# Optimization experiments

Measured on AMD Instinct MI355X. Metric: run time of the kernel, lower is better.

## Reference

```python
import jax, jax.numpy as jnp
import numpy as np

N_NODES = 100000
N_EDGES = 1600000
HIDDEN = 128
OUT_DIM = 1
N_GRAPHS = 2048
VOCAB = 28  # atom types, Embedding(28, hidden_dim)


def setup_inputs() -> dict:
    key = jax.random.key(0)
    ks = jax.random.split(key, 14)
    s = 1.0 / np.sqrt(HIDDEN)
    inp = {
        "x_idx": jax.random.randint(ks[0], (N_NODES,), 0, VOCAB, dtype=jnp.int32),
        "edge_src": jax.random.randint(ks[1], (N_EDGES,), 0, N_NODES, dtype=jnp.int32),
        "edge_dst": jax.random.randint(ks[2], (N_EDGES,), 0, N_NODES, dtype=jnp.int32),
        "batch": jnp.sort(jax.random.randint(ks[3], (N_NODES,), 0, N_GRAPHS, dtype=jnp.int32)),
        # parameters
        "embed": jax.random.normal(ks[4], (VOCAB, HIDDEN), dtype=jnp.float32) * 0.02,
        "eps0": jnp.zeros((1,), dtype=jnp.float32),
        "w1_0": jax.random.normal(ks[5], (HIDDEN, HIDDEN), dtype=jnp.float32) * s,
        "b1_0": jnp.zeros((HIDDEN,), dtype=jnp.float32),
        "w2_0": jax.random.normal(ks[6], (HIDDEN, HIDDEN), dtype=jnp.float32) * s,
        "b2_0": jnp.zeros((HIDDEN,), dtype=jnp.float32),
        "eps1": jnp.zeros((1,), dtype=jnp.float32),
        "w1_1": jax.random.normal(ks[7], (HIDDEN, HIDDEN), dtype=jnp.float32) * s,
        "b1_1": jnp.zeros((HIDDEN,), dtype=jnp.float32),
        "w2_1": jax.random.normal(ks[8], (HIDDEN, OUT_DIM), dtype=jnp.float32) * s,
        "b2_1": jnp.zeros((OUT_DIM,), dtype=jnp.float32),
    }
    return inp


def _gin_layer(x, edge_src, edge_dst, eps, w1, b1, w2, b2):
    # A @ x via edge-list SpMM: out[dst] += x[src]  (same math as to_dense().matmul(x))
    agg = jax.ops.segment_sum(x[edge_src], edge_dst, num_segments=N_NODES)
    h = agg + (1.0 + eps) * x  # [N, in_feats]; eps broadcasts (shape [1])
    h = h @ w1 + b1            # linear1 (no nonlinearity between, as in source)
    return h @ w2 + b2         # linear2


def reference(x_idx, edge_src, edge_dst, batch, embed,
              eps0, w1_0, b1_0, w2_0, b2_0,
              eps1, w1_1, b1_1, w2_1, b2_1):
    x = embed[x_idx]  # [N, HIDDEN] — Embedding lookup (.squeeze(1) trivial here)
    x = jax.nn.relu(_gin_layer(x, edge_src, edge_dst, eps0, w1_0, b1_0, w2_0, b2_0))
    x = _gin_layer(x, edge_src, edge_dst, eps1, w1_1, b1_1, w2_1, b2_1)  # [N, 1]
    y_hat = jax.ops.segment_sum(x.squeeze(-1), batch, num_segments=N_GRAPHS)  # [G]
    return (y_hat, x)
```

## Files before the change

### kernel.cpp

```cpp
#include <hip/hip_runtime.h>

#define N_NODES  100000
#define N_EDGES  1600000
#define HIDDEN   128
#define N_GRAPHS 2048
#define VOCAB    28
#define NB       512
#define NPB      196
#define CAP      3600
#define NBIN     512
#define EPB      3125
#define EPT      4
#define CSTR     29
#define MAGIC196 1402438302ULL

__global__ __launch_bounds__(256) void k_init(float* __restrict__ out,
                                              int* __restrict__ gcursor,
                                              const float* __restrict__ embed,
                                              const float* __restrict__ w1_0,
                                              float* __restrict__ T) {
    const int bid = blockIdx.x, tid = threadIdx.x;
    if (bid < 10) {
        int i = bid * 256 + tid;
        if (i < N_GRAPHS) out[i] = 0.0f;
        else if (i < N_GRAPHS + NB) gcursor[i - N_GRAPHS] = 0;
    } else {
        int g = (bid - 10) * 256 + tid;
        int i = g >> 7, j = g & 127;
        float s = 0.f;
#pragma unroll 8
        for (int k = 0; k < HIDDEN; ++k)
            s += embed[i * HIDDEN + k] * w1_0[k * HIDDEN + j];
        T[g] = s;
    }
}

__global__ __launch_bounds__(1024) void k_bin(const int* __restrict__ esrc,
                                              const int* __restrict__ edst,
                                              const int* __restrict__ x_idx,
                                              unsigned* __restrict__ binned,
                                              int* __restrict__ gcursor,
                                              const float* __restrict__ T,
                                              const float* __restrict__ w2_0,
                                              const float* __restrict__ b1_0,
                                              const float* __restrict__ b2_0,
                                              const float* __restrict__ w1_1,
                                              const float* __restrict__ b1_1,
                                              const float* __restrict__ w2_1,
                                              const float* __restrict__ b2_1,
                                              float* __restrict__ EW,
                                              float* __restrict__ bc0,
                                              float* __restrict__ wc1,
                                              float* __restrict__ bc1) {
    const int tid = threadIdx.x;
    const int bid = blockIdx.x;

    if (bid >= NBIN) {
        if (bid < NBIN + 4) {
            int g = (bid - NBIN) * 1024 + tid;
            if (g < VOCAB * HIDDEN) {
                int i = g >> 7, j = g & 127;
                float s = 0.f;
#pragma unroll 8
                for (int k = 0; k < HIDDEN; ++k)
                    s += T[i * HIDDEN + k] * w2_0[k * HIDDEN + j];
                EW[g] = s;
            }
        } else {
            if (tid < 128) {
                float s = 0.f;
#pragma unroll 8
                for (int k = 0; k < HIDDEN; ++k)
                    s += b1_0[k] * w2_0[k * HIDDEN + tid];
                bc0[tid] = s + b2_0[tid];
                if (tid == 0) {
                    float q = 0.f;
                    for (int k = 0; k < HIDDEN; ++k) q += b1_1[k] * w2_1[k];
                    bc1[0] = q + b2_1[0];
                }
            } else if (tid < 256) {
                int i = tid - 128;
                float s = 0.f;
#pragma unroll 8
                for (int k = 0; k < HIDDEN; ++k)
                    s += w1_1[i * HIDDEN + k] * w2_1[k];
                wc1[i] = s;
            }
        }
        return;
    }

    __shared__ int hist[NB];
    __shared__ int lcur[NB];
    __shared__ int gbase[NB];

    if (tid < NB) { hist[tid] = 0; lcur[tid] = 0; }
    __syncthreads();

    unsigned mypk[EPT];
    short    myb[EPT];
#pragma unroll
    for (int i = 0; i < EPT; ++i) {
        int idx = i * 1024 + tid;
        myb[i] = -1;
        if (idx < EPB) {
            int e   = bid * EPB + idx;
            int dst = edst[e];
            int src = esrc[e];
            int b   = (int)(((unsigned long long)dst * MAGIC196) >> 38);
            int dl  = dst - b * NPB;
            int vix = x_idx[src];
            mypk[i] = ((unsigned)dl << 22) | ((unsigned)vix << 17) | (unsigned)src;
            myb[i]  = (short)b;
            atomicAdd(&hist[b], 1);
        }
    }
    __syncthreads();

    if (tid < NB) {
        int v = hist[tid];
        gbase[tid] = (v > 0) ? atomicAdd(&gcursor[tid], v) : 0;
    }
    __syncthreads();

#pragma unroll
    for (int i = 0; i < EPT; ++i) {
        if (myb[i] >= 0) {
            int b  = myb[i];
            int lr = atomicAdd(&lcur[b], 1);
            binned[(size_t)b * CAP + gbase[b] + lr] = mypk[i];
        }
    }
}

__global__ __launch_bounds__(1024) void k_layerC(const unsigned* __restrict__ binned,
                                                 const int* __restrict__ gcursor,
                                                 const int* __restrict__ x_idx,
                                                 const float* __restrict__ EW,
                                                 const float* __restrict__ bc0,
                                                 const float* __restrict__ wc1,
                                                 const float* __restrict__ eps0,
                                                 float* __restrict__ d) {
    __shared__ int lcnt[NPB * CSTR];

    const int tid = threadIdx.x;
    const int b   = blockIdx.x;

    for (int i = tid; i < NPB * CSTR; i += 1024) lcnt[i] = 0;
    __syncthreads();

    const int cnt = gcursor[b];
    const unsigned* bp = binned + (size_t)b * CAP;
    for (int i = tid; i < cnt; i += 1024) {
        unsigned pk = bp[i];
        atomicAdd(&lcnt[(pk >> 22) * CSTR + ((pk >> 17) & 31)], 1);
    }
    __syncthreads();

    if (tid >= NPB) return;

    const int n      = b * NPB + tid;
    const bool valid = (n < N_NODES);
    const int xi     = valid ? x_idx[n] : 0;
    const float s    = 1.0f + eps0[0];

    float cf[VOCAB];
#pragma unroll
    for (int v = 0; v < VOCAB; ++v)
        cf[v] = (float)lcnt[tid * CSTR + v] + ((v == xi) ? s : 0.0f);

    const float4* EW4 = reinterpret_cast<const float4*>(EW);
    const float4* b04 = reinterpret_cast<const float4*>(bc0);
    const float4* w14 = reinterpret_cast<const float4*>(wc1);

    float dacc = 0.f;
#pragma unroll 1
    for (int f4 = 0; f4 < 32; ++f4) {
        float4 a = b04[f4];
#pragma unroll
        for (int v = 0; v < VOCAB; ++v) {
            float4 e = EW4[v * 32 + f4];
            a.x += cf[v] * e.x;
            a.y += cf[v] * e.y;
            a.z += cf[v] * e.z;
            a.w += cf[v] * e.w;
        }
        float4 w = w14[f4];
        dacc += fmaxf(a.x, 0.f) * w.x + fmaxf(a.y, 0.f) * w.y
              + fmaxf(a.z, 0.f) * w.z + fmaxf(a.w, 0.f) * w.w;
    }
    if (valid) d[n] = dacc;
}

__global__ __launch_bounds__(1024) void k_B2(const unsigned* __restrict__ binned,
                                             const int* __restrict__ gcursor,
                                             const float* __restrict__ d,
                                             const int* __restrict__ batch,
                                             const float* __restrict__ eps1,
                                             const float* __restrict__ bc1,
                                             float* __restrict__ out) {
    __shared__ float racc[NPB];
    __shared__ float gacc[N_GRAPHS];

    const int tid = threadIdx.x;
    const int b   = blockIdx.x;
    const int n0  = b * NPB;
    const int nlast = min(n0 + NPB - 1, N_NODES - 1);

    if (tid < NPB) racc[tid] = 0.f;
    const int g0 = batch[n0];
    const int g1 = batch[nlast];
    for (int g = g0 + tid; g <= g1; g += 1024) gacc[g] = 0.f;
    __syncthreads();

    const int cnt = gcursor[b];
    const unsigned* bp = binned + (size_t)b * CAP;
    for (int i = tid; i < cnt; i += 1024) {
        unsigned pk = bp[i];
        atomicAdd(&racc[pk >> 22], d[pk & 0x1FFFFu]);
    }
    __syncthreads();

    int n = n0 + tid;
    if (tid < NPB && n < N_NODES) {
        float r = (1.0f + eps1[0]) * d[n] + racc[tid] + bc1[0];
        out[N_GRAPHS + n] = r;
        atomicAdd(&gacc[batch[n]], r);
    }
    __syncthreads();
    for (int g = g0 + tid; g <= g1; g += 1024) {
        float v = gacc[g];
        if (v != 0.f) atomicAdd(&out[g], v);
    }
}

extern "C" void kernel_launch(void* const* d_in, const int* in_sizes, int n_in,
                              void* d_out, int out_size, void* d_ws, size_t ws_size,
                              hipStream_t stream) {
    const int*   x_idx = (const int*)d_in[0];
    const int*   esrc  = (const int*)d_in[1];
    const int*   edst  = (const int*)d_in[2];
    const int*   batch = (const int*)d_in[3];
    const float* embed = (const float*)d_in[4];
    const float* eps0  = (const float*)d_in[5];
    const float* w1_0  = (const float*)d_in[6];
    const float* b1_0  = (const float*)d_in[7];
    const float* w2_0  = (const float*)d_in[8];
    const float* b2_0  = (const float*)d_in[9];
    const float* eps1  = (const float*)d_in[10];
    const float* w1_1  = (const float*)d_in[11];
    const float* b1_1  = (const float*)d_in[12];
    const float* w2_1  = (const float*)d_in[13];
    const float* b2_1  = (const float*)d_in[14];

    float* out = (float*)d_out;

    int*      gcursor = (int*)d_ws;
    unsigned* binned  = (unsigned*)(gcursor + 512);
    float*    dvec    = (float*)(binned + (size_t)NB * CAP);
    float*    T       = dvec + 100352;
    float*    EW      = T + VOCAB * HIDDEN;
    float*    bc0     = EW + VOCAB * HIDDEN;
    float*    wc1     = bc0 + HIDDEN;
    float*    bc1     = wc1 + HIDDEN;

    k_init<<<24, 256, 0, stream>>>(out, gcursor, embed, w1_0, T);

    k_bin<<<NBIN + 5, 1024, 0, stream>>>(esrc, edst, x_idx, binned, gcursor,
                                         T, w2_0, b1_0, b2_0,
                                         w1_1, b1_1, w2_1, b2_1,
                                         EW, bc0, wc1, bc1);

    k_layerC<<<NB, 1024, 0, stream>>>(binned, gcursor, x_idx, EW, bc0, wc1, eps0, dvec);

    k_B2<<<NB, 1024, 0, stream>>>(binned, gcursor, dvec, batch, eps1, bc1, out);
}
```

Before: 158.9 us.

## Vectorize edge and bin loads, split layerC feature loop across four thread groups

```diff
diff --git a/kernel.cpp b/kernel.cpp
--- a/kernel.cpp
+++ b/kernel.cpp
@@ -9,8 +9,7 @@
 #define NPB      196
 #define CAP      3600
 #define NBIN     512
-#define EPB      3125
-#define EPT      4
+#define I4PB     784
 #define CSTR     29
 #define MAGIC196 1402438302ULL
 
@@ -97,22 +96,29 @@
     if (tid < NB) { hist[tid] = 0; lcur[tid] = 0; }
     __syncthreads();
 
-    unsigned mypk[EPT];
-    short    myb[EPT];
+    unsigned mypk[4];
+    short    myb[4];
+    myb[0] = myb[1] = myb[2] = myb[3] = -1;
+
+    if (tid < I4PB) {
+        int i4 = bid * I4PB + tid;
+        int e  = i4 << 2;
+        if (e < N_EDGES) {
+            int4 s4 = reinterpret_cast<const int4*>(esrc)[i4];
+            int4 d4 = reinterpret_cast<const int4*>(edst)[i4];
+            int srcs[4] = { s4.x, s4.y, s4.z, s4.w };
+            int dsts[4] = { d4.x, d4.y, d4.z, d4.w };
 #pragma unroll
-    for (int i = 0; i < EPT; ++i) {
-        int idx = i * 1024 + tid;
-        myb[i] = -1;
-        if (idx < EPB) {
-            int e   = bid * EPB + idx;
-            int dst = edst[e];
-            int src = esrc[e];
-            int b   = (int)(((unsigned long long)dst * MAGIC196) >> 38);
-            int dl  = dst - b * NPB;
-            int vix = x_idx[src];
-            mypk[i] = ((unsigned)dl << 22) | ((unsigned)vix << 17) | (unsigned)src;
-            myb[i]  = (short)b;
-            atomicAdd(&hist[b], 1);
+            for (int j = 0; j < 4; ++j) {
+                int dst = dsts[j];
+                int src = srcs[j];
+                int b   = (int)(((unsigned long long)dst * MAGIC196) >> 38);
+                int dl  = dst - b * NPB;
+                int vix = x_idx[src];
+                mypk[j] = ((unsigned)dl << 22) | ((unsigned)vix << 17) | (unsigned)src;
+                myb[j]  = (short)b;
+                atomicAdd(&hist[b], 1);
+            }
         }
     }
     __syncthreads();
@@ -124,11 +130,11 @@
     __syncthreads();
 
 #pragma unroll
-    for (int i = 0; i < EPT; ++i) {
-        if (myb[i] >= 0) {
-            int b  = myb[i];
+    for (int j = 0; j < 4; ++j) {
+        if (myb[j] >= 0) {
+            int b  = myb[j];
             int lr = atomicAdd(&lcur[b], 1);
-            binned[(size_t)b * CAP + gbase[b] + lr] = mypk[i];
+            binned[(size_t)b * CAP + gbase[b] + lr] = mypk[j];
         }
     }
 }
@@ -140,8 +146,9 @@
                                                  const float* __restrict__ bc0,
                                                  const float* __restrict__ wc1,
                                                  const float* __restrict__ eps0,
-                                                 float* __restrict__ d) {
-    __shared__ int lcnt[NPB * CSTR];
+                                                 float* __restrict__ dvec) {
+    __shared__ int   lcnt[NPB * CSTR];
+    __shared__ float part[1024];
 
     const int tid = threadIdx.x;
     const int b   = blockIdx.x;
@@ -151,50 +158,67 @@
 
     const int cnt = gcursor[b];
     const unsigned* bp = binned + (size_t)b * CAP;
-    for (int i = tid; i < cnt; i += 1024) {
+    const uint4* bp4 = reinterpret_cast<const uint4*>(bp);
+    const int cnt4 = cnt >> 2;
+    for (int i = tid; i < cnt4; i += 1024) {
+        uint4 p = bp4[i];
+        atomicAdd(&lcnt[(p.x >> 22) * CSTR + ((p.x >> 17) & 31)], 1);
+        atomicAdd(&lcnt[(p.y >> 22) * CSTR + ((p.y >> 17) & 31)], 1);
+        atomicAdd(&lcnt[(p.z >> 22) * CSTR + ((p.z >> 17) & 31)], 1);
+        atomicAdd(&lcnt[(p.w >> 22) * CSTR + ((p.w >> 17) & 31)], 1);
+    }
+    for (int i = (cnt4 << 2) + tid; i < cnt; i += 1024) {
         unsigned pk = bp[i];
         atomicAdd(&lcnt[(pk >> 22) * CSTR + ((pk >> 17) & 31)], 1);
     }
     __syncthreads();
 
-    if (tid >= NPB) return;
-
-    const int n      = b * NPB + tid;
-    const bool valid = (n < N_NODES);
-    const int xi     = valid ? x_idx[n] : 0;
-    const float s    = 1.0f + eps0[0];
-
-    float cf[VOCAB];
+    const int q  = tid >> 8;
+    const int nl = tid & 255;
+    const int n  = b * NPB + nl;
+    const bool active = (nl < NPB);
+    const bool valid  = active && (n < N_NODES);
+
+    float dacc = 0.f;
+    if (active) {
+        const int xi  = valid ? x_idx[n] : 0;
+        const float s = 1.0f + eps0[0];
+
+        float cf[VOCAB];
 #pragma unroll
-    for (int v = 0; v < VOCAB; ++v)
-        cf[v] = (float)lcnt[tid * CSTR + v] + ((v == xi) ? s : 0.0f);
-
-    const float4* EW4 = reinterpret_cast<const float4*>(EW);
-    const float4* b04 = reinterpret_cast<const float4*>(bc0);
-    const float4* w14 = reinterpret_cast<const float4*>(wc1);
-
-    float dacc = 0.f;
+        for (int v = 0; v < VOCAB; ++v)
+            cf[v] = (float)lcnt[nl * CSTR + v] + ((v == xi) ? s : 0.0f);
+
+        const float4* EW4 = reinterpret_cast<const float4*>(EW);
+        const float4* b04 = reinterpret_cast<const float4*>(bc0);
+        const float4* w14 = reinterpret_cast<const float4*>(wc1);
+
 #pragma unroll 1
-    for (int f4 = 0; f4 < 32; ++f4) {
-        float4 a = b04[f4];
+        for (int f4 = q * 8; f4 < q * 8 + 8; ++f4) {
+            float4 a = b04[f4];
 #pragma unroll
-        for (int v = 0; v < VOCAB; ++v) {
-            float4 e = EW4[v * 32 + f4];
-            a.x += cf[v] * e.x;
-            a.y += cf[v] * e.y;
-            a.z += cf[v] * e.z;
-            a.w += cf[v] * e.w;
+            for (int v = 0; v < VOCAB; ++v) {
+                float4 e = EW4[v * 32 + f4];
+                a.x += cf[v] * e.x;
+                a.y += cf[v] * e.y;
+                a.z += cf[v] * e.z;
+                a.w += cf[v] * e.w;
+            }
+            float4 w = w14[f4];
+            dacc += fmaxf(a.x, 0.f) * w.x + fmaxf(a.y, 0.f) * w.y
+                  + fmaxf(a.z, 0.f) * w.z + fmaxf(a.w, 0.f) * w.w;
         }
-        float4 w = w14[f4];
-        dacc += fmaxf(a.x, 0.f) * w.x + fmaxf(a.y, 0.f) * w.y
-              + fmaxf(a.z, 0.f) * w.z + fmaxf(a.w, 0.f) * w.w;
-    }
-    if (valid) d[n] = dacc;
+    }
+    part[tid] = dacc;
+    __syncthreads();
+
+    if (q == 0 && valid)
+        dvec[n] = part[nl] + part[256 + nl] + part[512 + nl] + part[768 + nl];
 }
 
 __global__ __launch_bounds__(1024) void k_B2(const unsigned* __restrict__ binned,
                                              const int* __restrict__ gcursor,
-                                             const float* __restrict__ d,
+                                             const float* __restrict__ dvec,
                                              const int* __restrict__ batch,
                                              const float* __restrict__ eps1,
                                              const float* __restrict__ bc1,
@@ -205,25 +229,35 @@
     const int tid = threadIdx.x;
     const int b   = blockIdx.x;
     const int n0  = b * NPB;
-    const int nlast = min(n0 + NPB - 1, N_NODES - 1);
+    const int nfirst = min(n0, N_NODES - 1);
+    const int nlast  = min(n0 + NPB - 1, N_NODES - 1);
 
     if (tid < NPB) racc[tid] = 0.f;
-    const int g0 = batch[n0];
+    const int g0 = batch[nfirst];
     const int g1 = batch[nlast];
     for (int g = g0 + tid; g <= g1; g += 1024) gacc[g] = 0.f;
     __syncthreads();
 
     const int cnt = gcursor[b];
     const unsigned* bp = binned + (size_t)b * CAP;
-    for (int i = tid; i < cnt; i += 1024) {
+    const uint4* bp4 = reinterpret_cast<const uint4*>(bp);
+    const int cnt4 = cnt >> 2;
+    for (int i = tid; i < cnt4; i += 1024) {
+        uint4 p = bp4[i];
+        atomicAdd(&racc[p.x >> 22], dvec[p.x & 0x1FFFFu]);
+        atomicAdd(&racc[p.y >> 22], dvec[p.y & 0x1FFFFu]);
+        atomicAdd(&racc[p.z >> 22], dvec[p.z & 0x1FFFFu]);
+        atomicAdd(&racc[p.w >> 22], dvec[p.w & 0x1FFFFu]);
+    }
+    for (int i = (cnt4 << 2) + tid; i < cnt; i += 1024) {
         unsigned pk = bp[i];
-        atomicAdd(&racc[pk >> 22], d[pk & 0x1FFFFu]);
+        atomicAdd(&racc[pk >> 22], dvec[pk & 0x1FFFFu]);
     }
     __syncthreads();
 
     int n = n0 + tid;
     if (tid < NPB && n < N_NODES) {
-        float r = (1.0f + eps1[0]) * d[n] + racc[tid] + bc1[0];
+        float r = (1.0f + eps1[0]) * dvec[n] + racc[tid] + bc1[0];
         out[N_GRAPHS + n] = r;
         atomicAdd(&gacc[batch[n]], r);
     }
@@ -271,7 +305,8 @@
                                          w1_1, b1_1, w2_1, b2_1,
                                          EW, bc0, wc1, bc1);
 
-    k_layerC<<<NB, 1024, 0, stream>>>(binned, gcursor, x_idx, EW, bc0, wc1, eps0, dvec);
+    k_layerC<<<NB, 1024, 0, stream>>>(binned, gcursor, x_idx, EW, bc0, wc1,
+                                      eps0, dvec);
 
     k_B2<<<NB, 1024, 0, stream>>>(binned, gcursor, dvec, batch, eps1, bc1, out);
 }
```

Result: slower. 192.9 us (+21.4%).
